# Optimization experiments

Hardware: AMD Instinct MI355X
Metric: run time of the kernel (lower is better)

## Reference

```python
import jax, jax.numpy as jnp
from jax import lax
import numpy as np
from jax.scipy.special import logsumexp

B, T, K = 64, 4096, 32

def setup_inputs() -> dict:
    key = jax.random.key(0)
    k1, k2, k3 = jax.random.split(key, 3)
    return {
        "emission_logp": jax.random.normal(k1, (B, T, K), dtype=jnp.float32),
        "log_pi": jax.random.normal(k2, (K,), dtype=jnp.float32),
        "log_A": jax.random.normal(k3, (K, K), dtype=jnp.float32),
    }

def reference(emission_logp, log_pi, log_A):
    b, t, k = emission_logp.shape
    lp = jax.nn.log_softmax(log_pi)            # [K]
    lA = jax.nn.log_softmax(log_A, axis=1)     # [K,K]
    em = jnp.swapaxes(emission_logp, 0, 1)     # [T,B,K] time-major for scan

    # forward recursion: alpha_t = logsumexp_i(alpha_{t-1,i} + A_{i,j}) + em_t
    a0 = lp[None, :] + em[0]                   # [B,K]
    def fstep(a_prev, e_t):
        a_new = logsumexp(a_prev[:, :, None] + lA[None, :, :], axis=1) + e_t
        return a_new, a_new
    _, alphas = lax.scan(fstep, a0, em[1:])
    alpha = jnp.concatenate([a0[None], alphas], axis=0)  # [T,B,K]

    # backward recursion: beta_t = logsumexp_j(beta_{t+1,j} + A_{i,j} + em_{t+1,j})
    bT = jnp.zeros((b, k), dtype=emission_logp.dtype)
    def bstep(b_next, e_next):
        b_new = logsumexp(b_next[:, None, :] + lA[None, :, :] + e_next[:, None, :], axis=2)
        return b_new, b_new
    _, betas = lax.scan(bstep, bT, em[1:], reverse=True)
    beta = jnp.concatenate([betas, bT[None]], axis=0)    # [T,B,K]

    log_gamma = alpha + beta
    log_gamma = log_gamma - logsumexp(log_gamma, axis=-1, keepdims=True)
    return jnp.swapaxes(log_gamma, 0, 1)       # [B,T,K]
```

## Files before the change

kernel.cpp:

```cpp
#include <hip/hip_runtime.h>

#define B_ 64
#define T_ 4096
#define K_ 32
#define C_ 128
#define L_ 32
#define NWARM 24
#define PFD 4
#define NBW (NWARM / PFD)
#define NBS (L_ / PFD)

typedef float f32x16 __attribute__((ext_vector_type(16)));
typedef float f32x4v __attribute__((ext_vector_type(4)));
typedef short s16x8 __attribute__((ext_vector_type(8)));

union W4 { unsigned u[4]; short s[8]; s16x8 v; };

__device__ __forceinline__ unsigned cvt_pk_bf16(float lo, float hi) {
  unsigned r;
  asm("v_cvt_pk_bf16_f32 %0, %1, %2" : "=v"(r) : "v"(lo), "v"(hi));
  return r;
}
__device__ __forceinline__ short f2bf(float x) {
  unsigned u = __float_as_uint(x);
  return (short)((u + 0x7FFFu + ((u >> 16) & 1u)) >> 16);
}
__device__ __forceinline__ float wmax32(float v) {
#pragma unroll
  for (int k = 16; k >= 1; k >>= 1) v = fmaxf(v, __shfl_xor(v, k, 32));
  return v;
}
__device__ __forceinline__ float wsum32(float v) {
#pragma unroll
  for (int k = 16; k >= 1; k >>= 1) v += __shfl_xor(v, k, 32);
  return v;
}

__global__ __launch_bounds__(1024) void prep_kernel(const float* __restrict__ log_pi,
                                                    const float* __restrict__ log_A,
                                                    float* __restrict__ eA,
                                                    float* __restrict__ lp) {
  int tid = (int)threadIdx.x;
  int i = tid >> 5, j = tid & 31;
  float a = log_A[i * K_ + j];
  float mm = wmax32(a);
  float e = __expf(a - mm);
  float S = wsum32(e);
  eA[i * K_ + j] = e / S;
  if (i == 0) {
    float v = log_pi[j];
    float m2 = wmax32(v);
    float ee = __expf(v - m2);
    float SS = wsum32(ee);
    lp[j] = v - m2 - __logf(SS);
  }
}

__global__ __launch_bounds__(128) void hmm_kernel(const float* __restrict__ em,
                                                  const float* __restrict__ eA,
                                                  const float* __restrict__ lp,
                                                  float* __restrict__ out) {
  __shared__ unsigned aw[L_ * 8 * 64];
  __shared__ unsigned bw[L_ * 8 * 64];
  const int bid = blockIdx.x;
  const int c = bid & (C_ - 1);
  const int g = bid >> 7;
  const int tid = (int)threadIdx.x;
  const int wv = tid >> 6;
  const int l = tid & 63;
  const int h = l >> 5;
  const int m = l & 31;
  const int b = (g << 5) + m;
  const int t0 = c * L_;
  const float* emb = em + (size_t)b * (T_ * K_) + 4 * h;

  W4 A1u, A2u, B1u, B2u;
#pragma unroll
  for (int r = 0; r < 8; ++r) {
    const int k1 = (r & 3) + 8 * (r >> 2) + 4 * h;
    const int k2 = k1 + 16;
    float a1 = (wv == 0) ? eA[k1 * K_ + m] : eA[m * K_ + k1];
    float a2 = (wv == 0) ? eA[k2 * K_ + m] : eA[m * K_ + k2];
    A1u.s[r] = f2bf(a1);
    A2u.s[r] = f2bf(a2);
  }
#pragma unroll
  for (int q = 0; q < 4; ++q) { B1u.u[q] = 0x3F803F80u; B2u.u[q] = 0x3F803F80u; }

  f32x16 zk;
#pragma unroll
  for (int r = 0; r < 16; ++r) zk[r] = 0.0f;

  f32x4v eb[PFD][4];

  if (wv == 0) {
    const int tstart = t0 - NWARM;
#pragma unroll
    for (int u = 0; u < PFD; ++u) {
      int t = tstart + u; if (t < 0) t = 0;
      const float* p = emb + (size_t)t * K_;
#pragma unroll
      for (int G = 0; G < 4; ++G) eb[u][G] = *(const f32x4v*)(p + 8 * G);
    }

#define FWD_STEP(BLK, U, SPH)                                                    \
    {                                                                            \
      const int t = (SPH) ? (t0 + (BLK) * PFD + (U)) : (tstart + (BLK) * PFD + (U)); \
      f32x16 acc = __builtin_amdgcn_mfma_f32_32x32x16_bf16(A1u.v, B1u.v, zk, 0, 0, 0); \
      acc = __builtin_amdgcn_mfma_f32_32x32x16_bf16(A2u.v, B2u.v, acc, 0, 0, 0); \
      if ((SPH) && c == 0 && (BLK) == 0 && (U) == 0) {                           \
        _Pragma("unroll")                                                        \
        for (int G = 0; G < 4; ++G) {                                            \
          f32x4v lv = *(const f32x4v*)(lp + 8 * G + 4 * h);                      \
          _Pragma("unroll")                                                      \
          for (int q = 0; q < 4; ++q) acc[4 * G + q] = __expf(lv[q]);            \
        }                                                                        \
      }                                                                          \
      float al[16];                                                              \
      _Pragma("unroll")                                                          \
      for (int G = 0; G < 4; ++G) {                                              \
        f32x4v ee = eb[U][G];                                                    \
        _Pragma("unroll")                                                        \
        for (int q = 0; q < 4; ++q) al[4 * G + q] = acc[4 * G + q] * __expf(ee[q]); \
      }                                                                          \
      { int tn = t + PFD; if (tn < 0) tn = 0; if (tn > T_ - 1) tn = T_ - 1;      \
        const float* p = emb + (size_t)tn * K_;                                  \
        _Pragma("unroll")                                                        \
        for (int G = 0; G < 4; ++G) eb[U][G] = *(const f32x4v*)(p + 8 * G); }    \
      if (((BLK) & 1) == 1 && (U) == 3) {                                        \
        float a0 = __shfl(al[0], m, 64);                                         \
        float rs = __builtin_amdgcn_rcpf(a0);                                    \
        _Pragma("unroll")                                                        \
        for (int r = 0; r < 16; ++r) al[r] *= rs;                                \
      }                                                                          \
      W4 nB1, nB2;                                                               \
      _Pragma("unroll")                                                          \
      for (int q = 0; q < 4; ++q) {                                              \
        nB1.u[q] = cvt_pk_bf16(al[2 * q], al[2 * q + 1]);                        \
        nB2.u[q] = cvt_pk_bf16(al[8 + 2 * q], al[8 + 2 * q + 1]);                \
      }                                                                          \
      if (SPH) {                                                                 \
        unsigned* base = aw + (t - t0) * (8 * 64) + h * 32 + m;                  \
        _Pragma("unroll")                                                        \
        for (int q = 0; q < 4; ++q) {                                            \
          base[q * 64] = nB1.u[q];                                               \
          base[(4 + q) * 64] = nB2.u[q];                                         \
        }                                                                        \
      }                                                                          \
      B1u = nB1; B2u = nB2;                                                      \
    }

    for (int blk = 0; blk < NBW; ++blk) {
      FWD_STEP(blk, 0, 0) FWD_STEP(blk, 1, 0) FWD_STEP(blk, 2, 0) FWD_STEP(blk, 3, 0)
    }
    for (int blk = 0; blk < NBS; ++blk) {
      FWD_STEP(blk, 0, 1) FWD_STEP(blk, 1, 1) FWD_STEP(blk, 2, 1) FWD_STEP(blk, 3, 1)
    }
  } else {
    const int tstart = t0 + L_ + NWARM - 1;
#pragma unroll
    for (int u = 0; u < PFD; ++u) {
      int t = tstart - u; if (t > T_ - 1) t = T_ - 1;
      const float* p = emb + (size_t)t * K_;
#pragma unroll
      for (int G = 0; G < 4; ++G) eb[u][G] = *(const f32x4v*)(p + 8 * G);
    }

#define BWD_STEP(BLK, U, SPH)                                                    \
    {                                                                            \
      const int t = (SPH) ? (t0 + L_ - 1 - (BLK) * PFD - (U))                    \
                          : (tstart - (BLK) * PFD - (U));                        \
      f32x16 acc = __builtin_amdgcn_mfma_f32_32x32x16_bf16(A1u.v, B1u.v, zk, 0, 0, 0); \
      acc = __builtin_amdgcn_mfma_f32_32x32x16_bf16(A2u.v, B2u.v, acc, 0, 0, 0); \
      if ((SPH) && c == C_ - 1 && (BLK) == 0 && (U) == 0) {                      \
        _Pragma("unroll")                                                        \
        for (int r = 0; r < 16; ++r) acc[r] = 1.0f;                              \
      }                                                                          \
      if (SPH) {                                                                 \
        W4 sB1, sB2;                                                             \
        _Pragma("unroll")                                                        \
        for (int q = 0; q < 4; ++q) {                                            \
          sB1.u[q] = cvt_pk_bf16(acc[2 * q], acc[2 * q + 1]);                    \
          sB2.u[q] = cvt_pk_bf16(acc[8 + 2 * q], acc[8 + 2 * q + 1]);            \
        }                                                                        \
        unsigned* base = bw + (t - t0) * (8 * 64) + h * 32 + m;                  \
        _Pragma("unroll")                                                        \
        for (int q = 0; q < 4; ++q) {                                            \
          base[q * 64] = sB1.u[q];                                               \
          base[(4 + q) * 64] = sB2.u[q];                                         \
        }                                                                        \
      }                                                                          \
      float al[16];                                                              \
      _Pragma("unroll")                                                          \
      for (int G = 0; G < 4; ++G) {                                              \
        f32x4v ee = eb[U][G];                                                    \
        _Pragma("unroll")                                                        \
        for (int q = 0; q < 4; ++q) al[4 * G + q] = acc[4 * G + q] * __expf(ee[q]); \
      }                                                                          \
      { int tn = t - PFD; if (tn < 0) tn = 0; if (tn > T_ - 1) tn = T_ - 1;      \
        const float* p = emb + (size_t)tn * K_;                                  \
        _Pragma("unroll")                                                        \
        for (int G = 0; G < 4; ++G) eb[U][G] = *(const f32x4v*)(p + 8 * G); }    \
      if (((BLK) & 1) == 1 && (U) == 3) {                                        \
        float a0 = __shfl(al[0], m, 64);                                         \
        float rs = __builtin_amdgcn_rcpf(a0);                                    \
        _Pragma("unroll")                                                        \
        for (int r = 0; r < 16; ++r) al[r] *= rs;                                \
      }                                                                          \
      W4 nB1, nB2;                                                               \
      _Pragma("unroll")                                                          \
      for (int q = 0; q < 4; ++q) {                                              \
        nB1.u[q] = cvt_pk_bf16(al[2 * q], al[2 * q + 1]);                        \
        nB2.u[q] = cvt_pk_bf16(al[8 + 2 * q], al[8 + 2 * q + 1]);                \
      }                                                                          \
      B1u = nB1; B2u = nB2;                                                      \
    }

    for (int blk = 0; blk < NBW; ++blk) {
      BWD_STEP(blk, 0, 0) BWD_STEP(blk, 1, 0) BWD_STEP(blk, 2, 0) BWD_STEP(blk, 3, 0)
    }
    for (int blk = 0; blk < NBS; ++blk) {
      BWD_STEP(blk, 0, 1) BWD_STEP(blk, 1, 1) BWD_STEP(blk, 2, 1) BWD_STEP(blk, 3, 1)
    }
  }

  __syncthreads();

  {
    float* outb = out + (size_t)b * (T_ * K_) + 4 * h;
    for (int rr = 0; rr < 16; ++rr) {
      const int row = wv * 16 + rr;
      const unsigned* pa = aw + row * (8 * 64) + h * 32 + m;
      const unsigned* pb = bw + row * (8 * 64) + h * 32 + m;
      float gg[16];
      float s = 0.0f;
#pragma unroll
      for (int w = 0; w < 8; ++w) {
        unsigned ua = pa[w * 64], ub = pb[w * 64];
        float a0 = __uint_as_float(ua << 16);
        float a1 = __uint_as_float(ua & 0xFFFF0000u);
        float b0 = __uint_as_float(ub << 16);
        float b1 = __uint_as_float(ub & 0xFFFF0000u);
        gg[2 * w] = a0 * b0;
        gg[2 * w + 1] = a1 * b1;
      }
#pragma unroll
      for (int r = 0; r < 16; ++r) s += gg[r];
      s += __shfl_xor(s, 32, 64);
      const float ls = __log2f(s);
      const int t = t0 + row;
      float* po = outb + (size_t)t * K_;
#pragma unroll
      for (int G = 0; G < 4; ++G) {
        f32x4v v;
#pragma unroll
        for (int q = 0; q < 4; ++q)
          v[q] = (__log2f(gg[4 * G + q]) - ls) * 0.6931471805599453f;
        *(f32x4v*)(po + 8 * G) = v;
      }
    }
  }
}

extern "C" void kernel_launch(void* const* d_in, const int* in_sizes, int n_in,
                              void* d_out, int out_size, void* d_ws, size_t ws_size,
                              hipStream_t stream) {
  const float* em = (const float*)d_in[0];
  const float* log_pi = (const float*)d_in[1];
  const float* log_A = (const float*)d_in[2];
  float* out = (float*)d_out;

  float* eA = (float*)d_ws;
  float* lp = eA + K_ * K_;

  prep_kernel<<<1, 1024, 0, stream>>>(log_pi, log_A, eA, lp);
  hmm_kernel<<<2 * C_, 128, 0, stream>>>(em, eA, lp, out);
}
```

Baseline: 37.19 us.

## Precompute exp(emission) as packed bf16 in MFMA layout via separate pre-pass kernel

```diff
diff --git a/kernel.cpp b/kernel.cpp
--- a/kernel.cpp
+++ b/kernel.cpp
@@ -5,9 +5,9 @@
 #define K_ 32
 #define C_ 128
 #define L_ 32
-#define NWARM 24
-#define PFD 4
-#define NBW (NWARM / PFD)
+#define W_ 32
+#define PFD 8
+#define NBW (W_ / PFD)
 #define NBS (L_ / PFD)
 
 typedef float f32x16 __attribute__((ext_vector_type(16)));
@@ -36,35 +36,63 @@
   return v;
 }
 
-__global__ __launch_bounds__(1024) void prep_kernel(const float* __restrict__ log_pi,
-                                                    const float* __restrict__ log_A,
-                                                    float* __restrict__ eA,
-                                                    float* __restrict__ lp) {
-  int tid = (int)threadIdx.x;
-  int i = tid >> 5, j = tid & 31;
-  float a = log_A[i * K_ + j];
-  float mm = wmax32(a);
-  float e = __expf(a - mm);
-  float S = wsum32(e);
-  eA[i * K_ + j] = e / S;
-  if (i == 0) {
-    float v = log_pi[j];
-    float m2 = wmax32(v);
-    float ee = __expf(v - m2);
-    float SS = wsum32(ee);
-    lp[j] = v - m2 - __logf(SS);
+__global__ __launch_bounds__(256) void pet_kernel(const float* __restrict__ em,
+                                                  const float* __restrict__ log_pi,
+                                                  const float* __restrict__ log_A,
+                                                  float* __restrict__ eA,
+                                                  float* __restrict__ lp,
+                                                  unsigned* __restrict__ peP) {
+  const int t = (int)blockIdx.x;
+  const int tid = (int)threadIdx.x;
+  if (t >= T_) {
+    const int i0 = tid >> 5, j = tid & 31;
+#pragma unroll
+    for (int rr = 0; rr < 4; ++rr) {
+      int i = i0 + 8 * rr;
+      float a = log_A[i * K_ + j];
+      float m = wmax32(a);
+      float e = __expf(a - m);
+      float S = wsum32(e);
+      eA[i * K_ + j] = e / S;
+    }
+    if (i0 == 0) {
+      float v = log_pi[j];
+      float m2 = wmax32(v);
+      float ee = __expf(v - m2);
+      float SS = wsum32(ee);
+      lp[j] = v - m2 - __logf(SS);
+    }
+    return;
   }
-}
-
-__global__ __launch_bounds__(128) void hmm_kernel(const float* __restrict__ em,
-                                                  const float* __restrict__ eA,
-                                                  const float* __restrict__ lp,
-                                                  float* __restrict__ out) {
+  __shared__ float tile[K_][B_];
+  const int b = tid >> 2, kq = tid & 3;
+  const float* p = em + (size_t)b * (T_ * K_) + (size_t)t * K_ + kq * 8;
+  f32x4v v0 = *(const f32x4v*)p;
+  f32x4v v1 = *(const f32x4v*)(p + 4);
+#pragma unroll
+  for (int q = 0; q < 4; ++q) tile[kq * 8 + q][b] = __expf(v0[q]);
+#pragma unroll
+  for (int q = 0; q < 4; ++q) tile[kq * 8 + 4 + q][b] = __expf(v1[q]);
+  __syncthreads();
+  unsigned* ob = peP + (size_t)t * 1024;
+#pragma unroll
+  for (int rr = 0; rr < 4; ++rr) {
+    int Wd = tid + 256 * rr;
+    int col = Wd & 63, wq = (Wd >> 6) & 7, h = Wd >> 9;
+    int s0 = 2 * (wq & 1) + 8 * (wq >> 1) + 4 * h;
+    ob[Wd] = cvt_pk_bf16(tile[s0][col], tile[s0 + 1][col]);
+  }
+}
+
+__global__ __launch_bounds__(256, 1) void hmm_kernel(const unsigned* __restrict__ peP,
+                                                     const float* __restrict__ eA,
+                                                     const float* __restrict__ lp,
+                                                     float* __restrict__ out) {
   __shared__ unsigned aw[L_ * 8 * 64];
   __shared__ unsigned bw[L_ * 8 * 64];
-  const int bid = blockIdx.x;
-  const int c = bid & (C_ - 1);
-  const int g = bid >> 7;
+  const int lid = ((int)blockIdx.x & 7) * 32 + ((int)blockIdx.x >> 3);
+  const int g = lid >> 7;
+  const int c = lid & (C_ - 1);
   const int tid = (int)threadIdx.x;
   const int wv = tid >> 6;
   const int l = tid & 63;
@@ -72,155 +100,158 @@
   const int m = l & 31;
   const int b = (g << 5) + m;
   const int t0 = c * L_;
-  const float* emb = em + (size_t)b * (T_ * K_) + 4 * h;
-
-  W4 A1u, A2u, B1u, B2u;
-#pragma unroll
-  for (int r = 0; r < 8; ++r) {
-    const int k1 = (r & 3) + 8 * (r >> 2) + 4 * h;
-    const int k2 = k1 + 16;
-    float a1 = (wv == 0) ? eA[k1 * K_ + m] : eA[m * K_ + k1];
-    float a2 = (wv == 0) ? eA[k2 * K_ + m] : eA[m * K_ + k2];
-    A1u.s[r] = f2bf(a1);
-    A2u.s[r] = f2bf(a2);
-  }
-#pragma unroll
-  for (int q = 0; q < 4; ++q) { B1u.u[q] = 0x3F803F80u; B2u.u[q] = 0x3F803F80u; }
+  const unsigned* pB = peP + (h << 9) + (g << 5) + m;
 
   f32x16 zk;
 #pragma unroll
   for (int r = 0; r < 16; ++r) zk[r] = 0.0f;
 
-  f32x4v eb[PFD][4];
-
-  if (wv == 0) {
-    const int tstart = t0 - NWARM;
-#pragma unroll
-    for (int u = 0; u < PFD; ++u) {
-      int t = tstart + u; if (t < 0) t = 0;
-      const float* p = emb + (size_t)t * K_;
-#pragma unroll
-      for (int G = 0; G < 4; ++G) eb[u][G] = *(const f32x4v*)(p + 8 * G);
-    }
+  if (wv < 2) {
+    W4 A1u, A2u, B1u, B2u;
+#pragma unroll
+    for (int r = 0; r < 8; ++r) {
+      const int k1 = (r & 3) + 8 * (r >> 2) + 4 * h;
+      const int k2 = k1 + 16;
+      float a1 = (wv == 0) ? eA[k1 * K_ + m] : eA[m * K_ + k1];
+      float a2 = (wv == 0) ? eA[k2 * K_ + m] : eA[m * K_ + k2];
+      A1u.s[r] = f2bf(a1);
+      A2u.s[r] = f2bf(a2);
+    }
+#pragma unroll
+    for (int q = 0; q < 4; ++q) { B1u.u[q] = 0x3F803F80u; B2u.u[q] = 0x3F803F80u; }
+
+    unsigned ring[PFD][8];
+
+    if (wv == 0) {
+      const int tstart = t0 - W_;
+#pragma unroll
+      for (int u = 0; u < PFD; ++u) {
+        int tt = tstart + u; if (tt < 0) tt = 0;
+        const unsigned* pp = pB + (size_t)tt * 1024;
+#pragma unroll
+        for (int w = 0; w < 8; ++w) ring[u][w] = pp[w * 64];
+      }
 
 #define FWD_STEP(BLK, U, SPH)                                                    \
-    {                                                                            \
-      const int t = (SPH) ? (t0 + (BLK) * PFD + (U)) : (tstart + (BLK) * PFD + (U)); \
-      f32x16 acc = __builtin_amdgcn_mfma_f32_32x32x16_bf16(A1u.v, B1u.v, zk, 0, 0, 0); \
-      acc = __builtin_amdgcn_mfma_f32_32x32x16_bf16(A2u.v, B2u.v, acc, 0, 0, 0); \
-      if ((SPH) && c == 0 && (BLK) == 0 && (U) == 0) {                           \
+      {                                                                          \
+        const int t = (SPH) ? (t0 + (BLK) * PFD + (U)) : (tstart + (BLK) * PFD + (U)); \
+        f32x16 acc = __builtin_amdgcn_mfma_f32_32x32x16_bf16(A1u.v, B1u.v, zk, 0, 0, 0); \
+        acc = __builtin_amdgcn_mfma_f32_32x32x16_bf16(A2u.v, B2u.v, acc, 0, 0, 0); \
+        if ((SPH) && c == 0 && (BLK) == 0 && (U) == 0) {                         \
+          _Pragma("unroll")                                                      \
+          for (int r = 0; r < 16; ++r)                                           \
+            acc[r] = __expf(lp[(r & 3) + 8 * (r >> 2) + 4 * h]);                 \
+        }                                                                        \
+        float al[16];                                                            \
         _Pragma("unroll")                                                        \
-        for (int G = 0; G < 4; ++G) {                                            \
-          f32x4v lv = *(const f32x4v*)(lp + 8 * G + 4 * h);                      \
-          _Pragma("unroll")                                                      \
-          for (int q = 0; q < 4; ++q) acc[4 * G + q] = __expf(lv[q]);            \
-        }                                                                        \
-      }                                                                          \
-      float al[16];                                                              \
-      _Pragma("unroll")                                                          \
-      for (int G = 0; G < 4; ++G) {                                              \
-        f32x4v ee = eb[U][G];                                                    \
-        _Pragma("unroll")                                                        \
-        for (int q = 0; q < 4; ++q) al[4 * G + q] = acc[4 * G + q] * __expf(ee[q]); \
-      }                                                                          \
-      { int tn = t + PFD; if (tn < 0) tn = 0; if (tn > T_ - 1) tn = T_ - 1;      \
-        const float* p = emb + (size_t)tn * K_;                                  \
-        _Pragma("unroll")                                                        \
-        for (int G = 0; G < 4; ++G) eb[U][G] = *(const f32x4v*)(p + 8 * G); }    \
-      if (((BLK) & 1) == 1 && (U) == 3) {                                        \
-        float a0 = __shfl(al[0], m, 64);                                         \
-        float rs = __builtin_amdgcn_rcpf(a0);                                    \
-        _Pragma("unroll")                                                        \
-        for (int r = 0; r < 16; ++r) al[r] *= rs;                                \
-      }                                                                          \
-      W4 nB1, nB2;                                                               \
-      _Pragma("unroll")                                                          \
-      for (int q = 0; q < 4; ++q) {                                              \
-        nB1.u[q] = cvt_pk_bf16(al[2 * q], al[2 * q + 1]);                        \
-        nB2.u[q] = cvt_pk_bf16(al[8 + 2 * q], al[8 + 2 * q + 1]);                \
-      }                                                                          \
-      if (SPH) {                                                                 \
-        unsigned* base = aw + (t - t0) * (8 * 64) + h * 32 + m;                  \
+        for (int w = 0; w < 8; ++w) {                                            \
+          unsigned P = ring[U][w];                                               \
+          al[2 * w]     = acc[2 * w]     * __uint_as_float(P << 16);             \
+          al[2 * w + 1] = acc[2 * w + 1] * __uint_as_float(P & 0xFFFF0000u);     \
+        }                                                                        \
+        { int tn = t + PFD; if (tn > T_ - 1) tn = T_ - 1; if (tn < 0) tn = 0;    \
+          const unsigned* pp = pB + (size_t)tn * 1024;                           \
+          _Pragma("unroll")                                                      \
+          for (int w = 0; w < 8; ++w) ring[U][w] = pp[w * 64]; }                 \
+        if ((U) == PFD - 1) {                                                    \
+          float a0 = __shfl(al[0], m, 64);                                       \
+          float rs = __builtin_amdgcn_rcpf(a0);                                  \
+          _Pragma("unroll")                                                      \
+          for (int r = 0; r < 16; ++r) al[r] *= rs;                              \
+        }                                                                        \
+        W4 nB1, nB2;                                                             \
         _Pragma("unroll")                                                        \
         for (int q = 0; q < 4; ++q) {                                            \
-          base[q * 64] = nB1.u[q];                                               \
-          base[(4 + q) * 64] = nB2.u[q];                                         \
-        }                                                                        \
-      }                                                                          \
-      B1u = nB1; B2u = nB2;                                                      \
-    }
-
-    for (int blk = 0; blk < NBW; ++blk) {
-      FWD_STEP(blk, 0, 0) FWD_STEP(blk, 1, 0) FWD_STEP(blk, 2, 0) FWD_STEP(blk, 3, 0)
-    }
-    for (int blk = 0; blk < NBS; ++blk) {
-      FWD_STEP(blk, 0, 1) FWD_STEP(blk, 1, 1) FWD_STEP(blk, 2, 1) FWD_STEP(blk, 3, 1)
-    }
-  } else {
-    const int tstart = t0 + L_ + NWARM - 1;
-#pragma unroll
-    for (int u = 0; u < PFD; ++u) {
-      int t = tstart - u; if (t > T_ - 1) t = T_ - 1;
-      const float* p = emb + (size_t)t * K_;
-#pragma unroll
-      for (int G = 0; G < 4; ++G) eb[u][G] = *(const f32x4v*)(p + 8 * G);
-    }
+          nB1.u[q] = cvt_pk_bf16(al[2 * q], al[2 * q + 1]);                      \
+          nB2.u[q] = cvt_pk_bf16(al[8 + 2 * q], al[8 + 2 * q + 1]);              \
+        }                                                                        \
+        if (SPH) {                                                               \
+          unsigned* base = aw + ((t - t0) << 9) + (h << 5) + m;                  \
+          _Pragma("unroll")                                                      \
+          for (int q = 0; q < 4; ++q) {                                          \
+            base[q * 64] = nB1.u[q];                                             \
+            base[(4 + q) * 64] = nB2.u[q];                                       \
+          }                                                                      \
+        }                                                                        \
+        B1u = nB1; B2u = nB2;                                                    \
+      }
+
+      for (int blk = 0; blk < NBW; ++blk) {
+        FWD_STEP(blk, 0, 0) FWD_STEP(blk, 1, 0) FWD_STEP(blk, 2, 0) FWD_STEP(blk, 3, 0)
+        FWD_STEP(blk, 4, 0) FWD_STEP(blk, 5, 0) FWD_STEP(blk, 6, 0) FWD_STEP(blk, 7, 0)
+      }
+      for (int blk = 0; blk < NBS; ++blk) {
+        FWD_STEP(blk, 0, 1) FWD_STEP(blk, 1, 1) FWD_STEP(blk, 2, 1) FWD_STEP(blk, 3, 1)
+        FWD_STEP(blk, 4, 1) FWD_STEP(blk, 5, 1) FWD_STEP(blk, 6, 1) FWD_STEP(blk, 7, 1)
+      }
+    } else {
+      const int tstart = t0 + L_ - 1 + W_;
+#pragma unroll
+      for (int u = 0; u < PFD; ++u) {
+        int tt = tstart - u; if (tt > T_ - 1) tt = T_ - 1;
+        const unsigned* pp = pB + (size_t)tt * 1024;
+#pragma unroll
+        for (int w = 0; w < 8; ++w) ring[u][w] = pp[w * 64];
+      }
 
 #define BWD_STEP(BLK, U, SPH)                                                    \
-    {                                                                            \
-      const int t = (SPH) ? (t0 + L_ - 1 - (BLK) * PFD - (U))                    \
-                          : (tstart - (BLK) * PFD - (U));                        \
-      f32x16 acc = __builtin_amdgcn_mfma_f32_32x32x16_bf16(A1u.v, B1u.v, zk, 0, 0, 0); \
-      acc = __builtin_amdgcn_mfma_f32_32x32x16_bf16(A2u.v, B2u.v, acc, 0, 0, 0); \
-      if ((SPH) && c == C_ - 1 && (BLK) == 0 && (U) == 0) {                      \
+      {                                                                          \
+        const int t = (SPH) ? (t0 + L_ - 1 - (BLK) * PFD - (U))                  \
+                            : (tstart - (BLK) * PFD - (U));                      \
+        f32x16 acc = __builtin_amdgcn_mfma_f32_32x32x16_bf16(A1u.v, B1u.v, zk, 0, 0, 0); \
+        acc = __builtin_amdgcn_mfma_f32_32x32x16_bf16(A2u.v, B2u.v, acc, 0, 0, 0); \
+        if ((SPH) && c == C_ - 1 && (BLK) == 0 && (U) == 0) {                    \
+          _Pragma("unroll")                                                      \
+          for (int r = 0; r < 16; ++r) acc[r] = 1.0f;                            \
+        }                                                                        \
+        if (SPH) {                                                               \
+          W4 sB1, sB2;                                                           \
+          _Pragma("unroll")                                                      \
+          for (int q = 0; q < 4; ++q) {                                          \
+            sB1.u[q] = cvt_pk_bf16(acc[2 * q], acc[2 * q + 1]);                  \
+            sB2.u[q] = cvt_pk_bf16(acc[8 + 2 * q], acc[8 + 2 * q + 1]);          \
+          }                                                                      \
+          unsigned* base = bw + ((t - t0) << 9) + (h << 5) + m;                  \
+          _Pragma("unroll")                                                      \
+          for (int q = 0; q < 4; ++q) {                                          \
+            base[q * 64] = sB1.u[q];                                             \
+            base[(4 + q) * 64] = sB2.u[q];                                       \
+          }                                                                      \
+        }                                                                        \
+        float al[16];                                                            \
         _Pragma("unroll")                                                        \
-        for (int r = 0; r < 16; ++r) acc[r] = 1.0f;                              \
-      }                                                                          \
-      if (SPH) {                                                                 \
-        W4 sB1, sB2;                                                             \
+        for (int w = 0; w < 8; ++w) {                                            \
+          unsigned P = ring[U][w];                                               \
+          al[2 * w]     = acc[2 * w]     * __uint_as_float(P << 16);             \
+          al[2 * w + 1] = acc[2 * w + 1] * __uint_as_float(P & 0xFFFF0000u);     \
+        }                                                                        \
+        { int tn = t - PFD; if (tn < 0) tn = 0; if (tn > T_ - 1) tn = T_ - 1;    \
+          const unsigned* pp = pB + (size_t)tn * 1024;                           \
+          _Pragma("unroll")                                                      \
+          for (int w = 0; w < 8; ++w) ring[U][w] = pp[w * 64]; }                 \
+        if ((U) == PFD - 1) {                                                    \
+          float a0 = __shfl(al[0], m, 64);                                       \
+          float rs = __builtin_amdgcn_rcpf(a0);                                  \
+          _Pragma("unroll")                                                      \
+          for (int r = 0; r < 16; ++r) al[r] *= rs;                              \
+        }                                                                        \
+        W4 nB1, nB2;                                                             \
         _Pragma("unroll")                                                        \
         for (int q = 0; q < 4; ++q) {                                            \
-          sB1.u[q] = cvt_pk_bf16(acc[2 * q], acc[2 * q + 1]);                    \
-          sB2.u[q] = cvt_pk_bf16(acc[8 + 2 * q], acc[8 + 2 * q + 1]);            \
-        }                                                                        \
-        unsigned* base = bw + (t - t0) * (8 * 64) + h * 32 + m;                  \
-        _Pragma("unroll")                                                        \
-        for (int q = 0; q < 4; ++q) {                                            \
-          base[q * 64] = sB1.u[q];                                               \
-          base[(4 + q) * 64] = sB2.u[q];                                         \
-        }                                                                        \
-      }                                                                          \
-      float al[16];                                                              \
-      _Pragma("unroll")                                                          \
-      for (int G = 0; G < 4; ++G) {                                              \
-        f32x4v ee = eb[U][G];                                                    \
-        _Pragma("unroll")                                                        \
-        for (int q = 0; q < 4; ++q) al[4 * G + q] = acc[4 * G + q] * __expf(ee[q]); \
-      }                                                                          \
-      { int tn = t - PFD; if (tn < 0) tn = 0; if (tn > T_ - 1) tn = T_ - 1;      \
-        const float* p = emb + (size_t)tn * K_;                                  \
-        _Pragma("unroll")                                                        \
-        for (int G = 0; G < 4; ++G) eb[U][G] = *(const f32x4v*)(p + 8 * G); }    \
-      if (((BLK) & 1) == 1 && (U) == 3) {                                        \
-        float a0 = __shfl(al[0], m, 64);                                         \
-        float rs = __builtin_amdgcn_rcpf(a0);                                    \
-        _Pragma("unroll")                                                        \
-        for (int r = 0; r < 16; ++r) al[r] *= rs;                                \
-      }                                                                          \
-      W4 nB1, nB2;                                                               \
-      _Pragma("unroll")                                                          \
-      for (int q = 0; q < 4; ++q) {                                              \
-        nB1.u[q] = cvt_pk_bf16(al[2 * q], al[2 * q + 1]);                        \
-        nB2.u[q] = cvt_pk_bf16(al[8 + 2 * q], al[8 + 2 * q + 1]);                \
-      }                                                                          \
-      B1u = nB1; B2u = nB2;                                                      \
-    }
-
-    for (int blk = 0; blk < NBW; ++blk) {
-      BWD_STEP(blk, 0, 0) BWD_STEP(blk, 1, 0) BWD_STEP(blk, 2, 0) BWD_STEP(blk, 3, 0)
-    }
-    for (int blk = 0; blk < NBS; ++blk) {
-      BWD_STEP(blk, 0, 1) BWD_STEP(blk, 1, 1) BWD_STEP(blk, 2, 1) BWD_STEP(blk, 3, 1)
+          nB1.u[q] = cvt_pk_bf16(al[2 * q], al[2 * q + 1]);                      \
+          nB2.u[q] = cvt_pk_bf16(al[8 + 2 * q], al[8 + 2 * q + 1]);              \
+        }                                                                        \
+        B1u = nB1; B2u = nB2;                                                    \
+      }
+
+      for (int blk = 0; blk < NBW; ++blk) {
+        BWD_STEP(blk, 0, 0) BWD_STEP(blk, 1, 0) BWD_STEP(blk, 2, 0) BWD_STEP(blk, 3, 0)
+        BWD_STEP(blk, 4, 0) BWD_STEP(blk, 5, 0) BWD_STEP(blk, 6, 0) BWD_STEP(blk, 7, 0)
+      }
+      for (int blk = 0; blk < NBS; ++blk) {
+        BWD_STEP(blk, 0, 1) BWD_STEP(blk, 1, 1) BWD_STEP(blk, 2, 1) BWD_STEP(blk, 3, 1)
+        BWD_STEP(blk, 4, 1) BWD_STEP(blk, 5, 1) BWD_STEP(blk, 6, 1) BWD_STEP(blk, 7, 1)
+      }
     }
   }
 
@@ -228,28 +259,23 @@
 
   {
     float* outb = out + (size_t)b * (T_ * K_) + 4 * h;
-    for (int rr = 0; rr < 16; ++rr) {
-      const int row = wv * 16 + rr;
-      const unsigned* pa = aw + row * (8 * 64) + h * 32 + m;
-      const unsigned* pb = bw + row * (8 * 64) + h * 32 + m;
+    for (int rr = 0; rr < 8; ++rr) {
+      const int row = wv * 8 + rr;
+      const unsigned* pa = aw + (row << 9) + (h << 5) + m;
+      const unsigned* pb = bw + (row << 9) + (h << 5) + m;
       float gg[16];
       float s = 0.0f;
 #pragma unroll
       for (int w = 0; w < 8; ++w) {
         unsigned ua = pa[w * 64], ub = pb[w * 64];
-        float a0 = __uint_as_float(ua << 16);
-        float a1 = __uint_as_float(ua & 0xFFFF0000u);
-        float b0 = __uint_as_float(ub << 16);
-        float b1 = __uint_as_float(ub & 0xFFFF0000u);
-        gg[2 * w] = a0 * b0;
-        gg[2 * w + 1] = a1 * b1;
+        gg[2 * w]     = __uint_as_float(ua << 16) * __uint_as_float(ub << 16);
+        gg[2 * w + 1] = __uint_as_float(ua & 0xFFFF0000u) * __uint_as_float(ub & 0xFFFF0000u);
       }
 #pragma unroll
       for (int r = 0; r < 16; ++r) s += gg[r];
       s += __shfl_xor(s, 32, 64);
       const float ls = __log2f(s);
-      const int t = t0 + row;
-      float* po = outb + (size_t)t * K_;
+      float* po = outb + (size_t)(t0 + row) * K_;
 #pragma unroll
       for (int G = 0; G < 4; ++G) {
         f32x4v v;
@@ -272,7 +298,8 @@
 
   float* eA = (float*)d_ws;
   float* lp = eA + K_ * K_;
-
-  prep_kernel<<<1, 1024, 0, stream>>>(log_pi, log_A, eA, lp);
-  hmm_kernel<<<2 * C_, 128, 0, stream>>>(em, eA, lp, out);
-}
+  unsigned* peP = (unsigned*)((char*)d_ws + 8192);
+
+  pet_kernel<<<T_ + 1, 256, 0, stream>>>(em, log_pi, log_A, eA, lp, peP);
+  hmm_kernel<<<2 * C_, 256, 0, stream>>>(peP, eA, lp, out);
+}
```

Measured after the change: 36.60 us. No clear change (-1.6%).

## Precompute exp-emissions as packed bf16 and stream them via producer warps

Applied to the files above, without the earlier changes.

```diff
diff --git a/kernel.cpp b/kernel.cpp
--- a/kernel.cpp
+++ b/kernel.cpp
@@ -5,10 +5,8 @@
 #define K_ 32
 #define C_ 128
 #define L_ 32
-#define NWARM 24
-#define PFD 4
-#define NBW (NWARM / PFD)
-#define NBS (L_ / PFD)
+#define W_ 32
+#define NPH 16
 
 typedef float f32x16 __attribute__((ext_vector_type(16)));
 typedef float f32x4v __attribute__((ext_vector_type(4)));
@@ -36,227 +34,246 @@
   return v;
 }
 
-__global__ __launch_bounds__(1024) void prep_kernel(const float* __restrict__ log_pi,
-                                                    const float* __restrict__ log_A,
-                                                    float* __restrict__ eA,
-                                                    float* __restrict__ lp) {
-  int tid = (int)threadIdx.x;
-  int i = tid >> 5, j = tid & 31;
-  float a = log_A[i * K_ + j];
-  float mm = wmax32(a);
-  float e = __expf(a - mm);
-  float S = wsum32(e);
-  eA[i * K_ + j] = e / S;
-  if (i == 0) {
-    float v = log_pi[j];
-    float m2 = wmax32(v);
-    float ee = __expf(v - m2);
-    float SS = wsum32(ee);
-    lp[j] = v - m2 - __logf(SS);
-  }
-}
-
-__global__ __launch_bounds__(128) void hmm_kernel(const float* __restrict__ em,
+__global__ __launch_bounds__(256) void pet_kernel(const float* __restrict__ em,
+                                                  const float* __restrict__ log_pi,
+                                                  const float* __restrict__ log_A,
+                                                  float* __restrict__ eA,
+                                                  float* __restrict__ lp,
+                                                  unsigned* __restrict__ peP) {
+  const int bid = (int)blockIdx.x;
+  const int tid = (int)threadIdx.x;
+  if (bid >= T_) {
+    const int i0 = tid >> 5, j = tid & 31;
+#pragma unroll
+    for (int rr = 0; rr < 4; ++rr) {
+      int i = i0 + 8 * rr;
+      float a = log_A[i * K_ + j];
+      float m = wmax32(a);
+      float e = __expf(a - m);
+      float S = wsum32(e);
+      eA[i * K_ + j] = e / S;
+    }
+    if (i0 == 0) {
+      float v = log_pi[j];
+      float m2 = wmax32(v);
+      float ee = __expf(v - m2);
+      float SS = wsum32(ee);
+      lp[j] = v - m2 - __logf(SS);
+    }
+    return;
+  }
+  const int t = ((bid & 7) << 9) + (bid >> 3);
+  __shared__ float tile[K_][B_];
+  const int b = tid >> 2, kq = tid & 3;
+  const float* p = em + (size_t)b * (T_ * K_) + (size_t)t * K_ + kq * 8;
+  f32x4v v0 = *(const f32x4v*)p;
+  f32x4v v1 = *(const f32x4v*)(p + 4);
+#pragma unroll
+  for (int q = 0; q < 4; ++q) tile[kq * 8 + q][b] = __expf(v0[q]);
+#pragma unroll
+  for (int q = 0; q < 4; ++q) tile[kq * 8 + 4 + q][b] = __expf(v1[q]);
+  __syncthreads();
+  unsigned* ob = peP + (size_t)t * 1024;
+#pragma unroll
+  for (int rr = 0; rr < 4; ++rr) {
+    int Wd = tid + 256 * rr;
+    int col = Wd & 63, wq = (Wd >> 6) & 7, hh = Wd >> 9;
+    int s0 = 2 * (wq & 1) + 8 * (wq >> 1) + 4 * hh;
+    ob[Wd] = cvt_pk_bf16(tile[s0][col], tile[s0 + 1][col]);
+  }
+}
+
+__global__ __launch_bounds__(256) void hmm_kernel(const unsigned* __restrict__ peP,
                                                   const float* __restrict__ eA,
                                                   const float* __restrict__ lp,
                                                   float* __restrict__ out) {
-  __shared__ unsigned aw[L_ * 8 * 64];
-  __shared__ unsigned bw[L_ * 8 * 64];
-  const int bid = blockIdx.x;
-  const int c = bid & (C_ - 1);
+  __shared__ __align__(16) unsigned aw[L_ * 512];
+  __shared__ __align__(16) unsigned bw[L_ * 512];
+  __shared__ __align__(16) unsigned prF[2 * 4 * 512];
+  __shared__ __align__(16) unsigned prB[2 * 4 * 512];
+
+  const int bid = (int)blockIdx.x;
+  const int c = ((bid & 7) << 4) + ((bid >> 3) & 15);
   const int g = bid >> 7;
   const int tid = (int)threadIdx.x;
   const int wv = tid >> 6;
   const int l = tid & 63;
   const int h = l >> 5;
   const int m = l & 31;
-  const int b = (g << 5) + m;
   const int t0 = c * L_;
-  const float* emb = em + (size_t)b * (T_ * K_) + 4 * h;
+
+  const int dsgn = (wv == 3) ? -1 : 1;
+  const int tbase = (wv == 3) ? (t0 + L_ - 1 + W_) : (t0 - W_);
+  const unsigned* gsrc = peP + (g << 5) + ((l >> 3) << 6) + ((l & 7) << 2);
+  uint4 pr[2][8];
 
   W4 A1u, A2u, B1u, B2u;
-#pragma unroll
-  for (int r = 0; r < 8; ++r) {
-    const int k1 = (r & 3) + 8 * (r >> 2) + 4 * h;
-    const int k2 = k1 + 16;
-    float a1 = (wv == 0) ? eA[k1 * K_ + m] : eA[m * K_ + k1];
-    float a2 = (wv == 0) ? eA[k2 * K_ + m] : eA[m * K_ + k2];
-    A1u.s[r] = f2bf(a1);
-    A2u.s[r] = f2bf(a2);
-  }
-#pragma unroll
-  for (int q = 0; q < 4; ++q) { B1u.u[q] = 0x3F803F80u; B2u.u[q] = 0x3F803F80u; }
-
+  unsigned rg[8];
   f32x16 zk;
 #pragma unroll
   for (int r = 0; r < 16; ++r) zk[r] = 0.0f;
 
-  f32x4v eb[PFD][4];
-
-  if (wv == 0) {
-    const int tstart = t0 - NWARM;
-#pragma unroll
-    for (int u = 0; u < PFD; ++u) {
-      int t = tstart + u; if (t < 0) t = 0;
-      const float* p = emb + (size_t)t * K_;
-#pragma unroll
-      for (int G = 0; G < 4; ++G) eb[u][G] = *(const f32x4v*)(p + 8 * G);
-    }
-
-#define FWD_STEP(BLK, U, SPH)                                                    \
-    {                                                                            \
-      const int t = (SPH) ? (t0 + (BLK) * PFD + (U)) : (tstart + (BLK) * PFD + (U)); \
-      f32x16 acc = __builtin_amdgcn_mfma_f32_32x32x16_bf16(A1u.v, B1u.v, zk, 0, 0, 0); \
-      acc = __builtin_amdgcn_mfma_f32_32x32x16_bf16(A2u.v, B2u.v, acc, 0, 0, 0); \
-      if ((SPH) && c == 0 && (BLK) == 0 && (U) == 0) {                           \
-        _Pragma("unroll")                                                        \
-        for (int G = 0; G < 4; ++G) {                                            \
-          f32x4v lv = *(const f32x4v*)(lp + 8 * G + 4 * h);                      \
-          _Pragma("unroll")                                                      \
-          for (int q = 0; q < 4; ++q) acc[4 * G + q] = __expf(lv[q]);            \
-        }                                                                        \
-      }                                                                          \
-      float al[16];                                                              \
-      _Pragma("unroll")                                                          \
-      for (int G = 0; G < 4; ++G) {                                              \
-        f32x4v ee = eb[U][G];                                                    \
-        _Pragma("unroll")                                                        \
-        for (int q = 0; q < 4; ++q) al[4 * G + q] = acc[4 * G + q] * __expf(ee[q]); \
-      }                                                                          \
-      { int tn = t + PFD; if (tn < 0) tn = 0; if (tn > T_ - 1) tn = T_ - 1;      \
-        const float* p = emb + (size_t)tn * K_;                                  \
-        _Pragma("unroll")                                                        \
-        for (int G = 0; G < 4; ++G) eb[U][G] = *(const f32x4v*)(p + 8 * G); }    \
-      if (((BLK) & 1) == 1 && (U) == 3) {                                        \
-        float a0 = __shfl(al[0], m, 64);                                         \
-        float rs = __builtin_amdgcn_rcpf(a0);                                    \
-        _Pragma("unroll")                                                        \
-        for (int r = 0; r < 16; ++r) al[r] *= rs;                                \
-      }                                                                          \
-      W4 nB1, nB2;                                                               \
-      _Pragma("unroll")                                                          \
-      for (int q = 0; q < 4; ++q) {                                              \
-        nB1.u[q] = cvt_pk_bf16(al[2 * q], al[2 * q + 1]);                        \
-        nB2.u[q] = cvt_pk_bf16(al[8 + 2 * q], al[8 + 2 * q + 1]);                \
-      }                                                                          \
-      if (SPH) {                                                                 \
-        unsigned* base = aw + (t - t0) * (8 * 64) + h * 32 + m;                  \
-        _Pragma("unroll")                                                        \
-        for (int q = 0; q < 4; ++q) {                                            \
-          base[q * 64] = nB1.u[q];                                               \
-          base[(4 + q) * 64] = nB2.u[q];                                         \
-        }                                                                        \
-      }                                                                          \
-      B1u = nB1; B2u = nB2;                                                      \
-    }
-
-    for (int blk = 0; blk < NBW; ++blk) {
-      FWD_STEP(blk, 0, 0) FWD_STEP(blk, 1, 0) FWD_STEP(blk, 2, 0) FWD_STEP(blk, 3, 0)
-    }
-    for (int blk = 0; blk < NBS; ++blk) {
-      FWD_STEP(blk, 0, 1) FWD_STEP(blk, 1, 1) FWD_STEP(blk, 2, 1) FWD_STEP(blk, 3, 1)
-    }
+  if (wv < 2) {
+#pragma unroll
+    for (int r = 0; r < 8; ++r) {
+      const int k1 = (r & 3) + 8 * (r >> 2) + 4 * h;
+      const int k2 = k1 + 16;
+      float a1 = (wv == 0) ? eA[k1 * K_ + m] : eA[m * K_ + k1];
+      float a2 = (wv == 0) ? eA[k2 * K_ + m] : eA[m * K_ + k2];
+      A1u.s[r] = f2bf(a1);
+      A2u.s[r] = f2bf(a2);
+    }
+#pragma unroll
+    for (int q = 0; q < 4; ++q) { B1u.u[q] = 0x3F803F80u; B2u.u[q] = 0x3F803F80u; }
   } else {
-    const int tstart = t0 + L_ + NWARM - 1;
-#pragma unroll
-    for (int u = 0; u < PFD; ++u) {
-      int t = tstart - u; if (t > T_ - 1) t = T_ - 1;
-      const float* p = emb + (size_t)t * K_;
-#pragma unroll
-      for (int G = 0; G < 4; ++G) eb[u][G] = *(const f32x4v*)(p + 8 * G);
-    }
-
-#define BWD_STEP(BLK, U, SPH)                                                    \
-    {                                                                            \
-      const int t = (SPH) ? (t0 + L_ - 1 - (BLK) * PFD - (U))                    \
-                          : (tstart - (BLK) * PFD - (U));                        \
-      f32x16 acc = __builtin_amdgcn_mfma_f32_32x32x16_bf16(A1u.v, B1u.v, zk, 0, 0, 0); \
-      acc = __builtin_amdgcn_mfma_f32_32x32x16_bf16(A2u.v, B2u.v, acc, 0, 0, 0); \
-      if ((SPH) && c == C_ - 1 && (BLK) == 0 && (U) == 0) {                      \
-        _Pragma("unroll")                                                        \
-        for (int r = 0; r < 16; ++r) acc[r] = 1.0f;                              \
-      }                                                                          \
-      if (SPH) {                                                                 \
-        W4 sB1, sB2;                                                             \
-        _Pragma("unroll")                                                        \
-        for (int q = 0; q < 4; ++q) {                                            \
-          sB1.u[q] = cvt_pk_bf16(acc[2 * q], acc[2 * q + 1]);                    \
-          sB2.u[q] = cvt_pk_bf16(acc[8 + 2 * q], acc[8 + 2 * q + 1]);            \
-        }                                                                        \
-        unsigned* base = bw + (t - t0) * (8 * 64) + h * 32 + m;                  \
-        _Pragma("unroll")                                                        \
-        for (int q = 0; q < 4; ++q) {                                            \
-          base[q * 64] = sB1.u[q];                                               \
-          base[(4 + q) * 64] = sB2.u[q];                                         \
-        }                                                                        \
-      }                                                                          \
-      float al[16];                                                              \
-      _Pragma("unroll")                                                          \
-      for (int G = 0; G < 4; ++G) {                                              \
-        f32x4v ee = eb[U][G];                                                    \
-        _Pragma("unroll")                                                        \
-        for (int q = 0; q < 4; ++q) al[4 * G + q] = acc[4 * G + q] * __expf(ee[q]); \
-      }                                                                          \
-      { int tn = t - PFD; if (tn < 0) tn = 0; if (tn > T_ - 1) tn = T_ - 1;      \
-        const float* p = emb + (size_t)tn * K_;                                  \
-        _Pragma("unroll")                                                        \
-        for (int G = 0; G < 4; ++G) eb[U][G] = *(const f32x4v*)(p + 8 * G); }    \
-      if (((BLK) & 1) == 1 && (U) == 3) {                                        \
-        float a0 = __shfl(al[0], m, 64);                                         \
-        float rs = __builtin_amdgcn_rcpf(a0);                                    \
-        _Pragma("unroll")                                                        \
-        for (int r = 0; r < 16; ++r) al[r] *= rs;                                \
-      }                                                                          \
-      W4 nB1, nB2;                                                               \
-      _Pragma("unroll")                                                          \
-      for (int q = 0; q < 4; ++q) {                                              \
-        nB1.u[q] = cvt_pk_bf16(al[2 * q], al[2 * q + 1]);                        \
-        nB2.u[q] = cvt_pk_bf16(al[8 + 2 * q], al[8 + 2 * q + 1]);                \
-      }                                                                          \
-      B1u = nB1; B2u = nB2;                                                      \
-    }
-
-    for (int blk = 0; blk < NBW; ++blk) {
-      BWD_STEP(blk, 0, 0) BWD_STEP(blk, 1, 0) BWD_STEP(blk, 2, 0) BWD_STEP(blk, 3, 0)
-    }
-    for (int blk = 0; blk < NBS; ++blk) {
-      BWD_STEP(blk, 0, 1) BWD_STEP(blk, 1, 1) BWD_STEP(blk, 2, 1) BWD_STEP(blk, 3, 1)
-    }
-  }
-
+    unsigned* ring = (wv == 2) ? prF : prB;
+#pragma unroll
+    for (int i = 0; i < 8; ++i) {
+      int tv = tbase + dsgn * (i >> 1);
+      tv = tv < 0 ? 0 : (tv > T_ - 1 ? T_ - 1 : tv);
+      pr[0][i] = *(const uint4*)(gsrc + (size_t)tv * 1024 + ((i & 1) << 9));
+    }
+#pragma unroll
+    for (int i = 0; i < 8; ++i)
+      *(uint4*)&ring[((i >> 1)) * 512 + ((i & 1) << 8) + 4 * l] = pr[0][i];
+#pragma unroll
+    for (int i = 0; i < 8; ++i) {
+      int tv = tbase + dsgn * (4 + (i >> 1));
+      tv = tv < 0 ? 0 : (tv > T_ - 1 ? T_ - 1 : tv);
+      pr[1][i] = *(const uint4*)(gsrc + (size_t)tv * 1024 + ((i & 1) << 9));
+    }
+  }
   __syncthreads();
 
+#define FSTEP(P, U)                                                            \
+  {                                                                            \
+    const int sg = 4 * (P) + (U);                                              \
+    _Pragma("unroll") for (int w = 0; w < 8; ++w)                              \
+      rg[w] = prF[(((P) & 1) * 4 + (U)) * 512 + h * 256 + w * 32 + m];         \
+    f32x16 acc = __builtin_amdgcn_mfma_f32_32x32x16_bf16(A1u.v, B1u.v, zk, 0, 0, 0); \
+    acc = __builtin_amdgcn_mfma_f32_32x32x16_bf16(A2u.v, B2u.v, acc, 0, 0, 0); \
+    if (sg == 32 && c == 0) {                                                  \
+      _Pragma("unroll") for (int r = 0; r < 16; ++r)                           \
+        acc[r] = __expf(lp[(r & 3) + 8 * (r >> 2) + 4 * h]);                   \
+    }                                                                          \
+    float al[16];                                                              \
+    _Pragma("unroll") for (int w = 0; w < 8; ++w) {                            \
+      al[2 * w]     = acc[2 * w]     * __uint_as_float(rg[w] << 16);           \
+      al[2 * w + 1] = acc[2 * w + 1] * __uint_as_float(rg[w] & 0xFFFF0000u);   \
+    }                                                                          \
+    if ((sg & 7) == 7) {                                                       \
+      float a0 = __shfl(al[0], m, 64);                                         \
+      float rs = __builtin_amdgcn_rcpf(a0);                                    \
+      _Pragma("unroll") for (int r = 0; r < 16; ++r) al[r] *= rs;              \
+    }                                                                          \
+    W4 nB1, nB2;                                                               \
+    _Pragma("unroll") for (int q = 0; q < 4; ++q) {                            \
+      nB1.u[q] = cvt_pk_bf16(al[2 * q], al[2 * q + 1]);                        \
+      nB2.u[q] = cvt_pk_bf16(al[8 + 2 * q], al[8 + 2 * q + 1]);                \
+    }                                                                          \
+    if (sg >= 32) {                                                            \
+      unsigned* bp = &aw[(sg - 32) * 512 + ((h << 5) + m) * 8];                \
+      *(uint4*)bp = *(uint4*)nB1.u;                                            \
+      *(uint4*)(bp + 4) = *(uint4*)nB2.u;                                      \
+    }                                                                          \
+    B1u = nB1; B2u = nB2;                                                      \
+  }
+
+#define BSTEP(P, U)                                                            \
+  {                                                                            \
+    const int sg = 4 * (P) + (U);                                              \
+    _Pragma("unroll") for (int w = 0; w < 8; ++w)                              \
+      rg[w] = prB[(((P) & 1) * 4 + (U)) * 512 + h * 256 + w * 32 + m];         \
+    f32x16 acc = __builtin_amdgcn_mfma_f32_32x32x16_bf16(A1u.v, B1u.v, zk, 0, 0, 0); \
+    acc = __builtin_amdgcn_mfma_f32_32x32x16_bf16(A2u.v, B2u.v, acc, 0, 0, 0); \
+    if (sg == 32 && c == C_ - 1) {                                             \
+      _Pragma("unroll") for (int r = 0; r < 16; ++r) acc[r] = 1.0f;            \
+    }                                                                          \
+    if (sg >= 32) {                                                            \
+      W4 s1, s2;                                                               \
+      _Pragma("unroll") for (int q = 0; q < 4; ++q) {                          \
+        s1.u[q] = cvt_pk_bf16(acc[2 * q], acc[2 * q + 1]);                     \
+        s2.u[q] = cvt_pk_bf16(acc[8 + 2 * q], acc[8 + 2 * q + 1]);             \
+      }                                                                        \
+      unsigned* bp = &bw[(63 - sg) * 512 + ((h << 5) + m) * 8];                \
+      *(uint4*)bp = *(uint4*)s1.u;                                             \
+      *(uint4*)(bp + 4) = *(uint4*)s2.u;                                       \
+    }                                                                          \
+    float al[16];                                                              \
+    _Pragma("unroll") for (int w = 0; w < 8; ++w) {                            \
+      al[2 * w]     = acc[2 * w]     * __uint_as_float(rg[w] << 16);           \
+      al[2 * w + 1] = acc[2 * w + 1] * __uint_as_float(rg[w] & 0xFFFF0000u);   \
+    }                                                                          \
+    if ((sg & 7) == 7) {                                                       \
+      float a0 = __shfl(al[0], m, 64);                                         \
+      float rs = __builtin_amdgcn_rcpf(a0);                                    \
+      _Pragma("unroll") for (int r = 0; r < 16; ++r) al[r] *= rs;              \
+    }                                                                          \
+    W4 nB1, nB2;                                                               \
+    _Pragma("unroll") for (int q = 0; q < 4; ++q) {                            \
+      nB1.u[q] = cvt_pk_bf16(al[2 * q], al[2 * q + 1]);                        \
+      nB2.u[q] = cvt_pk_bf16(al[8 + 2 * q], al[8 + 2 * q + 1]);                \
+    }                                                                          \
+    B1u = nB1; B2u = nB2;                                                      \
+  }
+
+#pragma unroll
+  for (int p = 0; p < NPH; ++p) {
+    if (wv == 0) {
+      FSTEP(p, 0) FSTEP(p, 1) FSTEP(p, 2) FSTEP(p, 3)
+    } else if (wv == 1) {
+      BSTEP(p, 0) BSTEP(p, 1) BSTEP(p, 2) BSTEP(p, 3)
+    } else {
+      unsigned* ring = (wv == 2) ? prF : prB;
+      if (p < NPH - 1) {
+#pragma unroll
+        for (int i = 0; i < 8; ++i)
+          *(uint4*)&ring[(((p + 1) & 1) * 4 + (i >> 1)) * 512 + ((i & 1) << 8) + 4 * l] =
+              pr[(p + 1) & 1][i];
+      }
+      if (p < NPH - 2) {
+#pragma unroll
+        for (int i = 0; i < 8; ++i) {
+          int tv = tbase + dsgn * (4 * (p + 2) + (i >> 1));
+          tv = tv < 0 ? 0 : (tv > T_ - 1 ? T_ - 1 : tv);
+          pr[p & 1][i] = *(const uint4*)(gsrc + (size_t)tv * 1024 + ((i & 1) << 9));
+        }
+      }
+    }
+    __syncthreads();
+  }
+
   {
-    float* outb = out + (size_t)b * (T_ * K_) + 4 * h;
-    for (int rr = 0; rr < 16; ++rr) {
-      const int row = wv * 16 + rr;
-      const unsigned* pa = aw + row * (8 * 64) + h * 32 + m;
-      const unsigned* pb = bw + row * (8 * 64) + h * 32 + m;
+#pragma unroll
+    for (int rr = 0; rr < 8; ++rr) {
+      const int row = wv * 8 + rr;
+      const unsigned* ap = &aw[row * 512 + ((h << 5) + m) * 8];
+      const unsigned* bp = &bw[row * 512 + ((h << 5) + m) * 8];
+      uint4 a1 = *(const uint4*)ap, a2 = *(const uint4*)(ap + 4);
+      uint4 b1 = *(const uint4*)bp, b2 = *(const uint4*)(bp + 4);
       float gg[16];
+#pragma unroll
+      for (int q = 0; q < 4; ++q) {
+        unsigned ua = ((const unsigned*)&a1)[q], ub = ((const unsigned*)&b1)[q];
+        gg[2 * q]     = __uint_as_float(ua << 16) * __uint_as_float(ub << 16);
+        gg[2 * q + 1] = __uint_as_float(ua & 0xFFFF0000u) * __uint_as_float(ub & 0xFFFF0000u);
+        unsigned va = ((const unsigned*)&a2)[q], vb = ((const unsigned*)&b2)[q];
+        gg[8 + 2 * q]     = __uint_as_float(va << 16) * __uint_as_float(vb << 16);
+        gg[8 + 2 * q + 1] = __uint_as_float(va & 0xFFFF0000u) * __uint_as_float(vb & 0xFFFF0000u);
+      }
       float s = 0.0f;
-#pragma unroll
-      for (int w = 0; w < 8; ++w) {
-        unsigned ua = pa[w * 64], ub = pb[w * 64];
-        float a0 = __uint_as_float(ua << 16);
-        float a1 = __uint_as_float(ua & 0xFFFF0000u);
-        float b0 = __uint_as_float(ub << 16);
-        float b1 = __uint_as_float(ub & 0xFFFF0000u);
-        gg[2 * w] = a0 * b0;
-        gg[2 * w + 1] = a1 * b1;
-      }
 #pragma unroll
       for (int r = 0; r < 16; ++r) s += gg[r];
       s += __shfl_xor(s, 32, 64);
       const float ls = __log2f(s);
-      const int t = t0 + row;
-      float* po = outb + (size_t)t * K_;
-#pragma unroll
-      for (int G = 0; G < 4; ++G) {
-        f32x4v v;
-#pragma unroll
-        for (int q = 0; q < 4; ++q)
-          v[q] = (__log2f(gg[4 * G + q]) - ls) * 0.6931471805599453f;
-        *(f32x4v*)(po + 8 * G) = v;
+      float* po = out + (size_t)((g << 5) + m) * (T_ * K_) + (size_t)(t0 + row) * K_;
+#pragma unroll
+      for (int w = 0; w < 8; ++w) {
+        const int k0 = 2 * (w & 1) + 8 * (w >> 1) + 4 * h;
+        float2 v;
+        v.x = (__log2f(gg[2 * w]) - ls) * 0.6931471805599453f;
+        v.y = (__log2f(gg[2 * w + 1]) - ls) * 0.6931471805599453f;
+        *(float2*)(po + k0) = v;
       }
     }
   }
@@ -272,7 +289,8 @@
 
   float* eA = (float*)d_ws;
   float* lp = eA + K_ * K_;
-
-  prep_kernel<<<1, 1024, 0, stream>>>(log_pi, log_A, eA, lp);
-  hmm_kernel<<<2 * C_, 128, 0, stream>>>(em, eA, lp, out);
-}
+  unsigned* peP = (unsigned*)((char*)d_ws + 8192);
+
+  pet_kernel<<<T_ + 1, 256, 0, stream>>>(em, log_pi, log_A, eA, lp, peP);
+  hmm_kernel<<<2 * C_, 256, 0, stream>>>(peP, eA, lp, out);
+}
```

Measured after the change: 41.79 us. 1.12x slower.
